# Optimization experiments

Measured on AMD Instinct MI355X. Metric: run time of the kernel, lower is better.

## Reference

```python
import jax, jax.numpy as jnp
import numpy as np

B, C_IN, C_OUT, N = 8, 256, 128, 4096
BN_EPS = 1e-5


def _conv1x1(w, b, t):
    # w: [out, in], t: [B, in, N] -> [B, out, N]
    return jnp.einsum('oc,bcn->bon', w, t) + b[None, :, None]


def setup_inputs() -> dict:
    key = jax.random.key(0)
    ks = jax.random.split(key, 11)
    s_in = 1.0 / np.sqrt(C_IN)
    s_out = 1.0 / np.sqrt(C_OUT)
    return {
        'x': jax.random.normal(ks[0], (B, C_IN, N), dtype=jnp.float32),
        'g_w': jax.random.normal(ks[1], (C_OUT, C_IN), dtype=jnp.float32) * s_in,
        'g_b': jax.random.normal(ks[2], (C_OUT,), dtype=jnp.float32) * s_in,
        'theta_w': jax.random.normal(ks[3], (C_OUT, C_IN), dtype=jnp.float32) * s_in,
        'theta_b': jax.random.normal(ks[4], (C_OUT,), dtype=jnp.float32) * s_in,
        'phi_w': jax.random.normal(ks[5], (C_OUT, C_IN), dtype=jnp.float32) * s_in,
        'phi_b': jax.random.normal(ks[6], (C_OUT,), dtype=jnp.float32) * s_in,
        'W_w': jax.random.normal(ks[7], (C_IN, C_OUT), dtype=jnp.float32) * s_out,
        'W_b': jax.random.normal(ks[8], (C_IN,), dtype=jnp.float32) * s_out,
        'bn_gamma': jax.random.uniform(ks[9], (C_IN,), dtype=jnp.float32),
        'bn_beta': jax.random.normal(ks[10], (C_IN,), dtype=jnp.float32) * 0.1,
    }


def reference(x, g_w, g_b, theta_w, theta_b, phi_w, phi_b, W_w, W_b, bn_gamma, bn_beta):
    n = x.shape[-1]
    g_x = _conv1x1(g_w, g_b, x)          # [B, Co, N]
    theta_x = _conv1x1(theta_w, theta_b, x)  # [B, Co, N]
    phi_x = _conv1x1(phi_w, phi_b, x)        # [B, Co, N]
    # f = theta_x^T @ phi_x, divided by N (no softmax) -> [B, N, N]
    f_div_c = jnp.einsum('bcn,bcm->bnm', theta_x, phi_x) / n
    # y[b,c,n] = sum_m f[b,n,m] * g_x[b,c,m]  -> already permuted to [B, Co, N]
    y = jnp.einsum('bnm,bcm->bcn', f_div_c, g_x)
    w_y = jnp.einsum('oc,bcn->bon', W_w, y) + W_b[None, :, None]  # [B, C_in, N]
    # BatchNorm1d, training mode: stats over (batch, spatial), biased variance
    mean = w_y.mean(axis=(0, 2), keepdims=True)
    var = w_y.var(axis=(0, 2), keepdims=True)
    w_y = (w_y - mean) * jax.lax.rsqrt(var + BN_EPS)
    w_y = w_y * bn_gamma[None, :, None] + bn_beta[None, :, None]
    return w_y + x  # generate=True residual
```

## Files before the change

kernel.cpp:

```cpp
#include <hip/hip_runtime.h>
#include <hip/hip_bf16.h>
#include <stdint.h>

#define BB   8
#define CIN  256
#define COUT 128
#define NN   4096

using f32x4  = __attribute__((ext_vector_type(4))) float;
using bf16x8 = __attribute__((ext_vector_type(8))) __bf16;
using u16x8  = __attribute__((ext_vector_type(8))) unsigned short;

static __device__ __forceinline__ unsigned short f2bf(float f) {
    unsigned int u = __builtin_bit_cast(unsigned int, f);
    u += 0x7FFFu + ((u >> 16) & 1u);
    return (unsigned short)(u >> 16);
}
static __device__ __forceinline__ float bf2f(unsigned short u) {
    return __builtin_bit_cast(float, (unsigned int)u << 16);
}
static __device__ __forceinline__ ushort4 pack4(float a, float b, float c, float d) {
    ushort4 r; r.x=f2bf(a); r.y=f2bf(b); r.z=f2bf(c); r.w=f2bf(d); return r;
}
#define MFMA(a,b,c) __builtin_amdgcn_mfma_f32_16x16x32_bf16((a),(b),(c),0,0,0)

static __device__ __forceinline__ int sw256(int r, int c) { return (r*256 + c) ^ ((r&7)<<3); }
static __device__ __forceinline__ int sw128(int r, int c) { return (r*128 + c) ^ ((r&7)<<3); }

__global__ __launch_bounds__(1024) void kA(
    const float* __restrict__ x,
    unsigned short* __restrict__ Sp, float* __restrict__ Rp)
{
    __shared__ __align__(16) unsigned short SH[65536];
    int bid = blockIdx.x;
    int b = bid >> 4, ch = bid & 15;
    int n0 = ch * 256;
    int t = threadIdx.x, lane = t & 63, wv = t >> 6;
    int lr = lane & 15, lg = lane >> 4;

    const float* xb = x + (size_t)b*CIN*NN + n0 + lane*4;
    #pragma unroll
    for (int g = 0; g < 2; ++g) {
        float4 v[8];
        #pragma unroll
        for (int i = 0; i < 8; ++i) {
            int c = wv*16 + g*8 + i;
            v[i] = *(const float4*)(xb + (size_t)c*NN);
        }
        #pragma unroll
        for (int i = 0; i < 8; ++i) {
            int c = wv*16 + g*8 + i;
            *(ushort4*)&SH[sw256(c, lane*4)] = pack4(v[i].x, v[i].y, v[i].z, v[i].w);
        }
    }
    __syncthreads();

    int wr = wv >> 2, wc = wv & 3;
    f32x4 acc[4][4];
    #pragma unroll
    for (int i = 0; i < 4; ++i)
        #pragma unroll
        for (int j = 0; j < 4; ++j) acc[i][j] = (f32x4){0.f,0.f,0.f,0.f};
    #pragma unroll
    for (int ks = 0; ks < 8; ++ks) {
        bf16x8 af[4], bfr[4];
        #pragma unroll
        for (int mi = 0; mi < 4; ++mi) {
            int row = wr*64 + mi*16 + lr;
            af[mi] = __builtin_bit_cast(bf16x8, *(const u16x8*)&SH[sw256(row, ks*32 + lg*8)]);
        }
        #pragma unroll
        for (int ni = 0; ni < 4; ++ni) {
            int row = wc*64 + ni*16 + lr;
            bfr[ni] = __builtin_bit_cast(bf16x8, *(const u16x8*)&SH[sw256(row, ks*32 + lg*8)]);
        }
        #pragma unroll
        for (int mi = 0; mi < 4; ++mi)
            #pragma unroll
            for (int ni = 0; ni < 4; ++ni)
                acc[mi][ni] = MFMA(af[mi], bfr[ni], acc[mi][ni]);
    }
    if (t < 256) {
        float s = 0.f;
        #pragma unroll
        for (int q = 0; q < 32; ++q) {
            u16x8 vv = *(const u16x8*)&SH[sw256(t, q*8)];
            #pragma unroll
            for (int e = 0; e < 8; ++e) s += bf2f(vv[e]);
        }
        Rp[bid*256 + t] = s;
    }
    __syncthreads();
    #pragma unroll
    for (int mi = 0; mi < 4; ++mi)
        #pragma unroll
        for (int ni = 0; ni < 4; ++ni)
            #pragma unroll
            for (int j = 0; j < 4; ++j) {
                int c1 = wr*64 + mi*16 + lg*4 + j;
                int c2 = wc*64 + ni*16 + lr;
                SH[sw256(c1, c2)] = f2bf(acc[mi][ni][j]);
            }
    __syncthreads();
    unsigned short* dst = Sp + (size_t)bid * 65536;
    #pragma unroll
    for (int i = t; i < 8192; i += 1024) {
        int row = i >> 5, q = i & 31;
        *(u16x8*)(dst + row*256 + ((q ^ (row&7)) * 8)) = *(const u16x8*)&SH[row*256 + q*8];
    }
}

__global__ __launch_bounds__(512) void kR(
    const unsigned short* __restrict__ Sp, const float* __restrict__ Rp,
    const float* __restrict__ Wwf, const float* __restrict__ gwf,
    const float* __restrict__ twf, const float* __restrict__ pwf,
    const float* __restrict__ gbv, const float* __restrict__ pbv, const float* __restrict__ tbv,
    unsigned short* __restrict__ Sbf, float* __restrict__ rv,
    unsigned short* __restrict__ Abf, unsigned short* __restrict__ CmT,
    float* __restrict__ a1, float* __restrict__ c1v, float* __restrict__ p2,
    float* __restrict__ params, float* __restrict__ stats)
{
    __shared__ __align__(16) unsigned short Ls[32768];
    __shared__ __align__(16) unsigned short Rs[32768];
    int bid = blockIdx.x;
    int t = threadIdx.x, lane = t & 63, wv = t >> 6;
    int lr = lane & 15, lg = lane >> 4;

    if (bid < 128) {
        int b = bid >> 4, sl = bid & 15;
        int base = sl*4096 + t*8;
        float s[8] = {0.f,0.f,0.f,0.f,0.f,0.f,0.f,0.f};
        #pragma unroll
        for (int i = 0; i < 16; ++i) {
            u16x8 v = *(const u16x8*)(Sp + (size_t)(b*16 + i)*65536 + base);
            #pragma unroll
            for (int e = 0; e < 8; ++e) s[e] += bf2f(v[e]);
        }
        u16x8 o;
        #pragma unroll
        for (int e = 0; e < 8; ++e) o[e] = f2bf(s[e]);
        *(u16x8*)(Sbf + (size_t)b*65536 + base) = o;
        return;
    }
    if (bid < 136) {
        int b = bid - 128;
        if (t < 256) {
            float s = 0.f;
            #pragma unroll
            for (int i = 0; i < 16; ++i) s += Rp[(b*16 + i)*256 + t];
            rv[b*256 + t] = s;
        }
        return;
    }

    if (bid == 136) {
        for (int i = t; i < 8192; i += 512) {
            int flat = i*4, r = flat >> 7, c = flat & 127;
            float4 f = *(const float4*)(Wwf + flat);
            *(ushort4*)&Ls[sw128(r, c)] = pack4(f.x, f.y, f.z, f.w);
        }
        {
            int c = lane * 4;  int k4 = wv * 4;
            #pragma unroll
            for (int rep = 0; rep < 4; ++rep) {
                int kb = rep*32 + k4;
                float4 f0 = *(const float4*)(gwf + (size_t)(kb+0)*256 + c);
                float4 f1 = *(const float4*)(gwf + (size_t)(kb+1)*256 + c);
                float4 f2 = *(const float4*)(gwf + (size_t)(kb+2)*256 + c);
                float4 f3 = *(const float4*)(gwf + (size_t)(kb+3)*256 + c);
                *(ushort4*)&Rs[sw128(c+0, kb)] = pack4(f0.x, f1.x, f2.x, f3.x);
                *(ushort4*)&Rs[sw128(c+1, kb)] = pack4(f0.y, f1.y, f2.y, f3.y);
                *(ushort4*)&Rs[sw128(c+2, kb)] = pack4(f0.z, f1.z, f2.z, f3.z);
                *(ushort4*)&Rs[sw128(c+3, kb)] = pack4(f0.w, f1.w, f2.w, f3.w);
            }
        }
        if (t < 512) stats[t] = 0.f;
    } else {
        {
            int c = lane * 4;  int k4 = wv * 4;
            #pragma unroll
            for (int rep = 0; rep < 4; ++rep) {
                int kb = rep*32 + k4;
                float4 f0 = *(const float4*)(twf + (size_t)(kb+0)*256 + c);
                float4 f1 = *(const float4*)(twf + (size_t)(kb+1)*256 + c);
                float4 f2 = *(const float4*)(twf + (size_t)(kb+2)*256 + c);
                float4 f3 = *(const float4*)(twf + (size_t)(kb+3)*256 + c);
                *(ushort4*)&Ls[sw128(c+0, kb)] = pack4(f0.x, f1.x, f2.x, f3.x);
                *(ushort4*)&Ls[sw128(c+1, kb)] = pack4(f0.y, f1.y, f2.y, f3.y);
                *(ushort4*)&Ls[sw128(c+2, kb)] = pack4(f0.z, f1.z, f2.z, f3.z);
                *(ushort4*)&Ls[sw128(c+3, kb)] = pack4(f0.w, f1.w, f2.w, f3.w);
                float4 g0 = *(const float4*)(pwf + (size_t)(kb+0)*256 + c);
                float4 g1 = *(const float4*)(pwf + (size_t)(kb+1)*256 + c);
                float4 g2 = *(const float4*)(pwf + (size_t)(kb+2)*256 + c);
                float4 g3 = *(const float4*)(pwf + (size_t)(kb+3)*256 + c);
                *(ushort4*)&Rs[sw128(c+0, kb)] = pack4(g0.x, g1.x, g2.x, g3.x);
                *(ushort4*)&Rs[sw128(c+1, kb)] = pack4(g0.y, g1.y, g2.y, g3.y);
                *(ushort4*)&Rs[sw128(c+2, kb)] = pack4(g0.z, g1.z, g2.z, g3.z);
                *(ushort4*)&Rs[sw128(c+3, kb)] = pack4(g0.w, g1.w, g2.w, g3.w);
            }
        }
    }
    __syncthreads();

    int wr = wv >> 2, wc = wv & 3;
    f32x4 acc[8][4];
    #pragma unroll
    for (int i = 0; i < 8; ++i)
        #pragma unroll
        for (int j = 0; j < 4; ++j) acc[i][j] = (f32x4){0.f,0.f,0.f,0.f};
    #pragma unroll
    for (int ks = 0; ks < 4; ++ks) {
        bf16x8 af[8], bfr[4];
        #pragma unroll
        for (int mi = 0; mi < 8; ++mi) {
            int r = wr*128 + mi*16 + lr;
            af[mi] = __builtin_bit_cast(bf16x8, *(const u16x8*)&Ls[sw128(r, ks*32 + lg*8)]);
        }
        #pragma unroll
        for (int ni = 0; ni < 4; ++ni) {
            int c = wc*64 + ni*16 + lr;
            bfr[ni] = __builtin_bit_cast(bf16x8, *(const u16x8*)&Rs[sw128(c, ks*32 + lg*8)]);
        }
        #pragma unroll
        for (int mi = 0; mi < 8; ++mi)
            #pragma unroll
            for (int ni = 0; ni < 4; ++ni)
                acc[mi][ni] = MFMA(af[mi], bfr[ni], acc[mi][ni]);
    }
    unsigned short* Dst = (bid == 136) ? Abf : CmT;
    #pragma unroll
    for (int mi = 0; mi < 8; ++mi)
        #pragma unroll
        for (int ni = 0; ni < 4; ++ni)
            #pragma unroll
            for (int j = 0; j < 4; ++j) {
                int r = wr*128 + mi*16 + lg*4 + j;
                int c = wc*64 + ni*16 + lr;
                Dst[r*256 + c] = f2bf(acc[mi][ni][j]);
            }

    if (bid == 136) {
        if (t < 256) {
            float s = 0.f;
            #pragma unroll
            for (int q = 0; q < 32; ++q) {
                float4 f = *(const float4*)(Wwf + (size_t)t*128 + q*4);
                s += f.x*gbv[q*4] + f.y*gbv[q*4+1] + f.z*gbv[q*4+2] + f.w*gbv[q*4+3];
            }
            a1[t] = s;
        }
    } else {
        if (t < 256) {
            float s1 = 0.f, s2 = 0.f;
            for (int k = 0; k < 128; ++k) {
                s1 += twf[(size_t)k*256 + t] * pbv[k];
                s2 += pwf[(size_t)k*256 + t] * tbv[k];
            }
            c1v[t] = s1; p2[t] = s2;
        }
        if (t < 64) {
            float v = pbv[t]*tbv[t] + pbv[t+64]*tbv[t+64];
            #pragma unroll
            for (int off = 1; off < 64; off <<= 1) v += __shfl_xor(v, off);
            if (t == 0) params[0] = v;
        }
    }
}

__global__ __launch_bounds__(512) void kE(
    const unsigned short* __restrict__ Sbf, const float* __restrict__ rv,
    const unsigned short* __restrict__ Abf, const unsigned short* __restrict__ CmT,
    const float* __restrict__ a1g, const float* __restrict__ c1vg, const float* __restrict__ p2g,
    const float* __restrict__ params, const float* __restrict__ Wbv,
    unsigned short* __restrict__ Ebf, float* __restrict__ fv, float* __restrict__ stats)
{
    __shared__ __align__(16) unsigned short Ybuf[16384];
    __shared__ __align__(16) unsigned short Ebuf[16384];
    __shared__ float r_l[256], p2_l[256], c1v_l[256], cr[256];
    __shared__ float a1_l[64], ar[64], Yp2[64], er[64], diag_l[64];
    __shared__ float rp2_s;
    int blk = blockIdx.x;
    int b = blk >> 2, obase = (blk & 3) * 64;
    int t = threadIdx.x, lane = t & 63, wv = t >> 6;
    int lr = lane & 15, lg = lane >> 4;
    const float invN = 1.0f/4096.0f;
    const unsigned short* Sb = Sbf + (size_t)b*65536;

    if (t < 256) {
        r_l[t] = rv[b*256 + t];
        p2_l[t] = p2g[t];
        c1v_l[t] = c1vg[t];
    } else if (t < 320) {
        a1_l[t - 256] = a1g[obase + (t - 256)];
    }
    __syncthreads();

    f32x4 acc[4][2];
    #pragma unroll
    for (int i = 0; i < 4; ++i) { acc[i][0] = (f32x4){0,0,0,0}; acc[i][1] = (f32x4){0,0,0,0}; }
    const unsigned short* Arow0 = Abf + (size_t)obase*256;
    #pragma unroll
    for (int ks = 0; ks < 8; ++ks) {
        bf16x8 a4[4], b2[2];
        #pragma unroll
        for (int mi = 0; mi < 4; ++mi)
            a4[mi] = __builtin_bit_cast(bf16x8, *(const u16x8*)(Arow0 + (size_t)(mi*16+lr)*256 + ks*32 + lg*8));
        #pragma unroll
        for (int ni = 0; ni < 2; ++ni)
            b2[ni] = __builtin_bit_cast(bf16x8, *(const u16x8*)(Sb + (size_t)(wv*32+ni*16+lr)*256 + ks*32 + lg*8));
        #pragma unroll
        for (int mi = 0; mi < 4; ++mi)
            #pragma unroll
            for (int ni = 0; ni < 2; ++ni)
                acc[mi][ni] = MFMA(a4[mi], b2[ni], acc[mi][ni]);
    }
    #pragma unroll
    for (int mi = 0; mi < 4; ++mi)
        #pragma unroll
        for (int ni = 0; ni < 2; ++ni)
            #pragma unroll
            for (int j = 0; j < 4; ++j) {
                int ol = mi*16 + lg*4 + j;
                int c2 = wv*32 + ni*16 + lr;
                Ybuf[ol*256 + (c2 ^ ((ol&7)<<3))] = f2bf(acc[mi][ni][j]);
            }
    __syncthreads();

    {
        int row = t >> 3, p8 = t & 7;
        float sA = 0.f, sY = 0.f;
        const unsigned short* Ar = Abf + (size_t)(obase + row)*256 + p8*32;
        #pragma unroll
        for (int q = 0; q < 4; ++q) {
            u16x8 av = *(const u16x8*)(Ar + q*8);
            #pragma unroll
            for (int e = 0; e < 8; ++e) {
                int c = p8*32 + q*8 + e;
                sA += bf2f(av[e]) * r_l[c];
                sY += bf2f(Ybuf[row*256 + (c ^ ((row&7)<<3))]) * p2_l[c];
            }
        }
        sA += __shfl_xor(sA, 1); sA += __shfl_xor(sA, 2); sA += __shfl_xor(sA, 4);
        sY += __shfl_xor(sY, 1); sY += __shfl_xor(sY, 2); sY += __shfl_xor(sY, 4);
        if (p8 == 0) { ar[row] = sA; Yp2[row] = sY; }
    }
    if (t < 256) {
        float s = 0.f;
        const unsigned short* Cr = CmT + (size_t)t*256;
        #pragma unroll
        for (int q = 0; q < 32; ++q) {
            u16x8 v = *(const u16x8*)(Cr + q*8);
            #pragma unroll
            for (int e = 0; e < 8; ++e) s += bf2f(v[e]) * r_l[q*8 + e];
        }
        cr[t] = s;
    }
    if (t < 64) {
        float v = r_l[t*4]*p2_l[t*4] + r_l[t*4+1]*p2_l[t*4+1]
                + r_l[t*4+2]*p2_l[t*4+2] + r_l[t*4+3]*p2_l[t*4+3];
        #pragma unroll
        for (int off = 1; off < 64; off <<= 1) v += __shfl_xor(v, off);
        if (t == 0) rp2_s = v;
    }
    __syncthreads();

    f32x4 accE[4][2];
    #pragma unroll
    for (int i = 0; i < 4; ++i) { accE[i][0] = (f32x4){0,0,0,0}; accE[i][1] = (f32x4){0,0,0,0}; }
    #pragma unroll
    for (int ks = 0; ks < 8; ++ks) {
        bf16x8 a4[4], b2[2];
        #pragma unroll
        for (int mi = 0; mi < 4; ++mi) {
            int ol = mi*16 + lr;
            a4[mi] = __builtin_bit_cast(bf16x8, *(const u16x8*)&Ybuf[ol*256 + ((ks*32 + lg*8) ^ ((ol&7)<<3))]);
        }
        #pragma unroll
        for (int ni = 0; ni < 2; ++ni)
            b2[ni] = __builtin_bit_cast(bf16x8, *(const u16x8*)(CmT + (size_t)(wv*32+ni*16+lr)*256 + ks*32 + lg*8));
        #pragma unroll
        for (int mi = 0; mi < 4; ++mi)
            #pragma unroll
            for (int ni = 0; ni < 2; ++ni)
                accE[mi][ni] = MFMA(a4[mi], b2[ni], accE[mi][ni]);
    }
    unsigned short* Eb = Ebf + (size_t)b*65536;
    #pragma unroll
    for (int mi = 0; mi < 4; ++mi)
        #pragma unroll
        for (int ni = 0; ni < 2; ++ni)
            #pragma unroll
            for (int j = 0; j < 4; ++j) {
                int ol = mi*16 + lg*4 + j;
                int cp = wv*32 + ni*16 + lr;
                float e = accE[mi][ni][j]*invN + a1_l[ol]*invN*cr[cp]
                        + (invN*ar[ol] + a1_l[ol])*c1v_l[cp];
                unsigned short eb = f2bf(e);
                Ebuf[ol*256 + (cp ^ ((ol&7)<<3))] = eb;
                Eb[(size_t)(obase + ol)*256 + cp] = eb;
            }
    __syncthreads();

    float f_reg = 0.f;
    {
        int row = t >> 3, p8 = t & 7;
        float s = 0.f;
        #pragma unroll
        for (int q = 0; q < 4; ++q)
            #pragma unroll
            for (int e = 0; e < 8; ++e) {
                int c = p8*32 + q*8 + e;
                s += bf2f(Ebuf[row*256 + (c ^ ((row&7)<<3))]) * r_l[c];
            }
        s += __shfl_xor(s, 1); s += __shfl_xor(s, 2); s += __shfl_xor(s, 4);
        if (p8 == 0) er[row] = s;
    }
    if (t < 64) {
        diag_l[t] = 0.f;
        float sg = params[0];
        f_reg = invN*(Yp2[t] + a1_l[t]*rp2_s + ar[t]*sg) + a1_l[t]*sg + Wbv[obase + t];
        fv[b*256 + obase + t] = f_reg;
    }
    __syncthreads();

    f32x4 accZ[4][2];
    #pragma unroll
    for (int i = 0; i < 4; ++i) { accZ[i][0] = (f32x4){0,0,0,0}; accZ[i][1] = (f32x4){0,0,0,0}; }
    #pragma unroll
    for (int ks = 0; ks < 8; ++ks) {
        bf16x8 a4[4], b2[2];
        #pragma unroll
        for (int mi = 0; mi < 4; ++mi) {
            int ol = mi*16 + lr;
            a4[mi] = __builtin_bit_cast(bf16x8, *(const u16x8*)&Ebuf[ol*256 + ((ks*32 + lg*8) ^ ((ol&7)<<3))]);
        }
        #pragma unroll
        for (int ni = 0; ni < 2; ++ni)
            b2[ni] = __builtin_bit_cast(bf16x8, *(const u16x8*)(Sb + (size_t)(wv*32+ni*16+lr)*256 + ks*32 + lg*8));
        #pragma unroll
        for (int mi = 0; mi < 4; ++mi)
            #pragma unroll
            for (int ni = 0; ni < 2; ++ni)
                accZ[mi][ni] = MFMA(a4[mi], b2[ni], accZ[mi][ni]);
    }
    #pragma unroll
    for (int mi = 0; mi < 4; ++mi)
        #pragma unroll
        for (int j = 0; j < 4; ++j) {
            int ol = mi*16 + lg*4 + j;
            float s = 0.f;
            #pragma unroll
            for (int ni = 0; ni < 2; ++ni) {
                int c2 = wv*32 + ni*16 + lr;
                s += accZ[mi][ni][j] * bf2f(Ebuf[ol*256 + (c2 ^ ((ol&7)<<3))]);
            }
            s += __shfl_xor(s, 1); s += __shfl_xor(s, 2);
            s += __shfl_xor(s, 4); s += __shfl_xor(s, 8);
            if (lr == 0) atomicAdd(&diag_l[ol], s);
        }
    __syncthreads();

    if (t < 64) {
        int o = obase + t;
        atomicAdd(&stats[o], er[t] + 4096.0f*f_reg);
        atomicAdd(&stats[256 + o], diag_l[t] + 2.0f*f_reg*er[t] + 4096.0f*f_reg*f_reg);
    }
}

__global__ __launch_bounds__(512) void kF(
    const float* __restrict__ x, const unsigned short* __restrict__ Ebf,
    const float* __restrict__ fv, const float* __restrict__ stats,
    const float* __restrict__ gamma, const float* __restrict__ beta,
    float* __restrict__ out)
{
    __shared__ __align__(16) unsigned short Xs[128*256];
    __shared__ float scale_l[256], shift_l[256];
    int b = blockIdx.x >> 5, n0 = (blockIdx.x & 31) * 128;
    int t = threadIdx.x, lane = t & 63, wv = t >> 6, lr = lane & 15, lg = lane >> 4;
    const float inv = 1.0f / 32768.0f;
    if (t < 256) {
        float mu  = stats[t] * inv;
        float var = stats[256 + t] * inv - mu*mu;
        float sc  = gamma[t] * rsqrtf(var + 1e-5f);
        scale_l[t] = sc;
        shift_l[t] = (fv[b*256 + t] - mu) * sc + beta[t];
    }
    {
        int nq = (t & 31) * 4, c0 = (t >> 5) * 4;
        const float* xb = x + (size_t)b*CIN*NN + n0 + nq;
        #pragma unroll
        for (int h = 0; h < 2; ++h) {
            float4 f[8];
            #pragma unroll
            for (int p = 0; p < 2; ++p) {
                int c = (h*2 + p)*64 + c0;
                const float* xp = xb + (size_t)c*NN;
                f[p*4+0] = *(const float4*)(xp);
                f[p*4+1] = *(const float4*)(xp + NN);
                f[p*4+2] = *(const float4*)(xp + 2*NN);
                f[p*4+3] = *(const float4*)(xp + 3*NN);
            }
            #pragma unroll
            for (int p = 0; p < 2; ++p) {
                int c = (h*2 + p)*64 + c0;
                *(ushort4*)&Xs[(nq+0)*256 + (c ^ (((nq+0)&7)<<3))] = pack4(f[p*4].x, f[p*4+1].x, f[p*4+2].x, f[p*4+3].x);
                *(ushort4*)&Xs[(nq+1)*256 + (c ^ (((nq+1)&7)<<3))] = pack4(f[p*4].y, f[p*4+1].y, f[p*4+2].y, f[p*4+3].y);
                *(ushort4*)&Xs[(nq+2)*256 + (c ^ (((nq+2)&7)<<3))] = pack4(f[p*4].z, f[p*4+1].z, f[p*4+2].z, f[p*4+3].z);
                *(ushort4*)&Xs[(nq+3)*256 + (c ^ (((nq+3)&7)<<3))] = pack4(f[p*4].w, f[p*4+1].w, f[p*4+2].w, f[p*4+3].w);
            }
        }
    }
    __syncthreads();

    int wn = wv >> 2, wo = wv & 3;
    int nb = wn*64, ob = wo*64;
    const unsigned short* Eb = Ebf + (size_t)b*65536;
    f32x4 acc[4][4];
    #pragma unroll
    for (int i = 0; i < 4; ++i)
        #pragma unroll
        for (int j = 0; j < 4; ++j) acc[i][j] = (f32x4){0,0,0,0};

    #pragma unroll
    for (int ks = 0; ks < 8; ++ks) {
        bf16x8 xf[4], ef[4];
        #pragma unroll
        for (int ni = 0; ni < 4; ++ni) {
            int n = nb + ni*16 + lr;
            xf[ni] = __builtin_bit_cast(bf16x8, *(const u16x8*)&Xs[(n*256 + ks*32 + lg*8) ^ ((n&7)<<3)]);
        }
        #pragma unroll
        for (int oi = 0; oi < 4; ++oi) {
            int o = ob + oi*16 + lr;
            ef[oi] = __builtin_bit_cast(bf16x8, *(const u16x8*)(Eb + (size_t)o*256 + ks*32 + lg*8));
        }
        #pragma unroll
        for (int oi = 0; oi < 4; ++oi)
            #pragma unroll
            for (int ni = 0; ni < 4; ++ni)
                acc[oi][ni] = MFMA(ef[oi], xf[ni], acc[oi][ni]);
    }

    float* op = out + (size_t)b*CIN*NN + n0;
    #pragma unroll
    for (int oi = 0; oi < 4; ++oi) {
        #pragma unroll
        for (int j = 0; j < 4; ++j) {
            int o = ob + oi*16 + lg*4 + j;
            float sc = scale_l[o], sh = shift_l[o];
            #pragma unroll
            for (int ni = 0; ni < 4; ++ni) {
                int n = nb + ni*16 + lr;
                float val = acc[oi][ni][j]*sc + sh + bf2f(Xs[(n*256 + (o ^ ((n&7)<<3)))]);
                op[(size_t)o*NN + n] = val;
            }
        }
    }
}

extern "C" void kernel_launch(void* const* d_in, const int* in_sizes, int n_in,
                              void* d_out, int out_size, void* d_ws, size_t ws_size,
                              hipStream_t stream)
{
    (void)in_sizes; (void)n_in; (void)out_size; (void)ws_size;
    const float* x     = (const float*)d_in[0];
    const float* gw    = (const float*)d_in[1];
    const float* gb    = (const float*)d_in[2];
    const float* tw    = (const float*)d_in[3];
    const float* tb    = (const float*)d_in[4];
    const float* pw    = (const float*)d_in[5];
    const float* pb    = (const float*)d_in[6];
    const float* Ww    = (const float*)d_in[7];
    const float* Wb    = (const float*)d_in[8];
    const float* gamma = (const float*)d_in[9];
    const float* beta  = (const float*)d_in[10];
    float* out = (float*)d_out;

    char* ws = (char*)d_ws;
    unsigned short* Sp  = (unsigned short*)(ws + 0);
    float* Rp           = (float*)(ws + 16777216);
    unsigned short* Sbf = (unsigned short*)(ws + 16908288);
    float* rv           = (float*)(ws + 17956864);
    unsigned short* Abf = (unsigned short*)(ws + 17965056);
    unsigned short* CmT = (unsigned short*)(ws + 18096128);
    unsigned short* Ebf = (unsigned short*)(ws + 18227200);
    float* fv           = (float*)(ws + 19275776);
    float* a1           = (float*)(ws + 19283968);
    float* c1v          = (float*)(ws + 19284992);
    float* p2           = (float*)(ws + 19286016);
    float* params       = (float*)(ws + 19287040);
    float* stats        = (float*)(ws + 19287104);

    kA<<<128, 1024, 0, stream>>>(x, Sp, Rp);
    kR<<<138, 512,  0, stream>>>(Sp, Rp, Ww, gw, tw, pw, gb, pb, tb,
                                 Sbf, rv, Abf, CmT, a1, c1v, p2, params, stats);
    kE<<<32,  512,  0, stream>>>(Sbf, rv, Abf, CmT, a1, c1v, p2, params, Wb, Ebf, fv, stats);
    kF<<<256, 512,  0, stream>>>(x, Ebf, fv, stats, gamma, beta, out);
}
```

Before: 91.38 us.

## Halve per-block N tiles in kA and kF to double grid size

kA now handles 128 spatial columns per 512-thread block (256 blocks), computing the 256x256 Gram partial with an 8-wave layout and writing it back in two half-passes through a halved LDS buffer. kF processes 64 columns per block over 512 blocks with half the accumulators. The intent is to fill more CUs on the 256-CU device, since the old 128- and 256-block grids left many CUs idle. In exchange kA writes twice as many partial Gram matrices (double the Sp workspace), and kR's reduction reads 32 partials instead of 16, which adds memory traffic.

```diff
diff --git a/kernel.cpp b/kernel.cpp
--- a/kernel.cpp
+++ b/kernel.cpp
@@ -27,86 +27,91 @@
 static __device__ __forceinline__ int sw256(int r, int c) { return (r*256 + c) ^ ((r&7)<<3); }
 static __device__ __forceinline__ int sw128(int r, int c) { return (r*128 + c) ^ ((r&7)<<3); }
 
-__global__ __launch_bounds__(1024) void kA(
+__global__ __launch_bounds__(512) void kA(
     const float* __restrict__ x,
     unsigned short* __restrict__ Sp, float* __restrict__ Rp)
 {
-    __shared__ __align__(16) unsigned short SH[65536];
+    __shared__ __align__(16) unsigned short SH[32768];
     int bid = blockIdx.x;
-    int b = bid >> 4, ch = bid & 15;
-    int n0 = ch * 256;
+    int b = bid >> 5, ch = bid & 31;
+    int n0 = ch * 128;
     int t = threadIdx.x, lane = t & 63, wv = t >> 6;
     int lr = lane & 15, lg = lane >> 4;
 
-    const float* xb = x + (size_t)b*CIN*NN + n0 + lane*4;
-    #pragma unroll
-    for (int g = 0; g < 2; ++g) {
-        float4 v[8];
-        #pragma unroll
-        for (int i = 0; i < 8; ++i) {
-            int c = wv*16 + g*8 + i;
-            v[i] = *(const float4*)(xb + (size_t)c*NN);
-        }
-        #pragma unroll
-        for (int i = 0; i < 8; ++i) {
-            int c = wv*16 + g*8 + i;
-            *(ushort4*)&SH[sw256(c, lane*4)] = pack4(v[i].x, v[i].y, v[i].z, v[i].w);
-        }
-    }
-    __syncthreads();
-
-    int wr = wv >> 2, wc = wv & 3;
-    f32x4 acc[4][4];
+    {
+        int n4 = (t & 31) * 4;
+        int c0 = t >> 5;
+        const float* xb = x + (size_t)b*CIN*NN + n0 + n4;
+        float4 v[16];
+        #pragma unroll
+        for (int i = 0; i < 16; ++i)
+            v[i] = *(const float4*)(xb + (size_t)(c0 + i*16)*NN);
+        #pragma unroll
+        for (int i = 0; i < 16; ++i) {
+            int c = c0 + i*16;
+            *(ushort4*)&SH[sw128(c, n4)] = pack4(v[i].x, v[i].y, v[i].z, v[i].w);
+        }
+    }
+    __syncthreads();
+
+    int wr = wv >> 1, wc = wv & 1;
+    f32x4 acc[4][8];
     #pragma unroll
     for (int i = 0; i < 4; ++i)
         #pragma unroll
-        for (int j = 0; j < 4; ++j) acc[i][j] = (f32x4){0.f,0.f,0.f,0.f};
-    #pragma unroll
-    for (int ks = 0; ks < 8; ++ks) {
-        bf16x8 af[4], bfr[4];
+        for (int j = 0; j < 8; ++j) acc[i][j] = (f32x4){0.f,0.f,0.f,0.f};
+    #pragma unroll
+    for (int ks = 0; ks < 4; ++ks) {
+        bf16x8 af[4], bfr[8];
         #pragma unroll
         for (int mi = 0; mi < 4; ++mi) {
             int row = wr*64 + mi*16 + lr;
-            af[mi] = __builtin_bit_cast(bf16x8, *(const u16x8*)&SH[sw256(row, ks*32 + lg*8)]);
-        }
-        #pragma unroll
-        for (int ni = 0; ni < 4; ++ni) {
-            int row = wc*64 + ni*16 + lr;
-            bfr[ni] = __builtin_bit_cast(bf16x8, *(const u16x8*)&SH[sw256(row, ks*32 + lg*8)]);
+            af[mi] = __builtin_bit_cast(bf16x8, *(const u16x8*)&SH[sw128(row, ks*32 + lg*8)]);
+        }
+        #pragma unroll
+        for (int ni = 0; ni < 8; ++ni) {
+            int row = wc*128 + ni*16 + lr;
+            bfr[ni] = __builtin_bit_cast(bf16x8, *(const u16x8*)&SH[sw128(row, ks*32 + lg*8)]);
         }
         #pragma unroll
         for (int mi = 0; mi < 4; ++mi)
             #pragma unroll
-            for (int ni = 0; ni < 4; ++ni)
+            for (int ni = 0; ni < 8; ++ni)
                 acc[mi][ni] = MFMA(af[mi], bfr[ni], acc[mi][ni]);
     }
     if (t < 256) {
         float s = 0.f;
         #pragma unroll
-        for (int q = 0; q < 32; ++q) {
-            u16x8 vv = *(const u16x8*)&SH[sw256(t, q*8)];
+        for (int q = 0; q < 16; ++q) {
+            u16x8 vv = *(const u16x8*)&SH[sw128(t, q*8)];
             #pragma unroll
             for (int e = 0; e < 8; ++e) s += bf2f(vv[e]);
         }
         Rp[bid*256 + t] = s;
     }
-    __syncthreads();
-    #pragma unroll
-    for (int mi = 0; mi < 4; ++mi)
-        #pragma unroll
-        for (int ni = 0; ni < 4; ++ni)
-            #pragma unroll
-            for (int j = 0; j < 4; ++j) {
-                int c1 = wr*64 + mi*16 + lg*4 + j;
-                int c2 = wc*64 + ni*16 + lr;
-                SH[sw256(c1, c2)] = f2bf(acc[mi][ni][j]);
-            }
-    __syncthreads();
+
     unsigned short* dst = Sp + (size_t)bid * 65536;
     #pragma unroll
-    for (int i = t; i < 8192; i += 1024) {
-        int row = i >> 5, q = i & 31;
-        *(u16x8*)(dst + row*256 + ((q ^ (row&7)) * 8)) = *(const u16x8*)&SH[row*256 + q*8];
+    for (int p = 0; p < 2; ++p) {
+        __syncthreads();
+        if (wc == p) {
+            #pragma unroll
+            for (int mi = 0; mi < 4; ++mi)
+                #pragma unroll
+                for (int ni = 0; ni < 8; ++ni)
+                    #pragma unroll
+                    for (int j = 0; j < 4; ++j) {
+                        int c1 = wr*64 + mi*16 + lg*4 + j;
+                        int c2l = ni*16 + lr;
+                        SH[sw128(c1, c2l)] = f2bf(acc[mi][ni][j]);
+                    }
+        }
+        __syncthreads();
+        #pragma unroll
+        for (int i = t; i < 4096; i += 512) {
+            int row = i >> 4, q = i & 15;
+            *(u16x8*)(dst + row*256 + p*128 + ((q ^ (row&7)) * 8)) = *(const u16x8*)&SH[row*128 + q*8];
+        }
     }
 }
 
@@ -131,8 +136,8 @@
         int base = sl*4096 + t*8;
         float s[8] = {0.f,0.f,0.f,0.f,0.f,0.f,0.f,0.f};
         #pragma unroll
-        for (int i = 0; i < 16; ++i) {
-            u16x8 v = *(const u16x8*)(Sp + (size_t)(b*16 + i)*65536 + base);
+        for (int i = 0; i < 32; ++i) {
+            u16x8 v = *(const u16x8*)(Sp + (size_t)(b*32 + i)*65536 + base);
             #pragma unroll
             for (int e = 0; e < 8; ++e) s[e] += bf2f(v[e]);
         }
@@ -147,7 +152,7 @@
         if (t < 256) {
             float s = 0.f;
             #pragma unroll
-            for (int i = 0; i < 16; ++i) s += Rp[(b*16 + i)*256 + t];
+            for (int i = 0; i < 32; ++i) s += Rp[(b*32 + i)*256 + t];
             rv[b*256 + t] = s;
         }
         return;
@@ -473,9 +478,9 @@
     const float* __restrict__ gamma, const float* __restrict__ beta,
     float* __restrict__ out)
 {
-    __shared__ __align__(16) unsigned short Xs[128*256];
+    __shared__ __align__(16) unsigned short Xs[64*256];
     __shared__ float scale_l[256], shift_l[256];
-    int b = blockIdx.x >> 5, n0 = (blockIdx.x & 31) * 128;
+    int b = blockIdx.x >> 6, n0 = (blockIdx.x & 63) * 64;
     int t = threadIdx.x, lane = t & 63, wv = t >> 6, lr = lane & 15, lg = lane >> 4;
     const float inv = 1.0f / 32768.0f;
     if (t < 256) {
@@ -486,46 +491,42 @@
         shift_l[t] = (fv[b*256 + t] - mu) * sc + beta[t];
     }
     {
-        int nq = (t & 31) * 4, c0 = (t >> 5) * 4;
-        const float* xb = x + (size_t)b*CIN*NN + n0 + nq;
-        #pragma unroll
-        for (int h = 0; h < 2; ++h) {
-            float4 f[8];
-            #pragma unroll
-            for (int p = 0; p < 2; ++p) {
-                int c = (h*2 + p)*64 + c0;
-                const float* xp = xb + (size_t)c*NN;
-                f[p*4+0] = *(const float4*)(xp);
-                f[p*4+1] = *(const float4*)(xp + NN);
-                f[p*4+2] = *(const float4*)(xp + 2*NN);
-                f[p*4+3] = *(const float4*)(xp + 3*NN);
-            }
-            #pragma unroll
-            for (int p = 0; p < 2; ++p) {
-                int c = (h*2 + p)*64 + c0;
-                *(ushort4*)&Xs[(nq+0)*256 + (c ^ (((nq+0)&7)<<3))] = pack4(f[p*4].x, f[p*4+1].x, f[p*4+2].x, f[p*4+3].x);
-                *(ushort4*)&Xs[(nq+1)*256 + (c ^ (((nq+1)&7)<<3))] = pack4(f[p*4].y, f[p*4+1].y, f[p*4+2].y, f[p*4+3].y);
-                *(ushort4*)&Xs[(nq+2)*256 + (c ^ (((nq+2)&7)<<3))] = pack4(f[p*4].z, f[p*4+1].z, f[p*4+2].z, f[p*4+3].z);
-                *(ushort4*)&Xs[(nq+3)*256 + (c ^ (((nq+3)&7)<<3))] = pack4(f[p*4].w, f[p*4+1].w, f[p*4+2].w, f[p*4+3].w);
-            }
+        int n4 = (t & 15) * 4;
+        int cb = (t >> 4) * 4;
+        const float* xb = x + (size_t)b*CIN*NN + n0 + n4;
+        float4 f[8];
+        #pragma unroll
+        for (int p = 0; p < 2; ++p) {
+            int c = p*128 + cb;
+            const float* xp = xb + (size_t)c*NN;
+            f[p*4+0] = *(const float4*)(xp);
+            f[p*4+1] = *(const float4*)(xp + NN);
+            f[p*4+2] = *(const float4*)(xp + 2*NN);
+            f[p*4+3] = *(const float4*)(xp + 3*NN);
+        }
+        #pragma unroll
+        for (int p = 0; p < 2; ++p) {
+            int c = p*128 + cb;
+            *(ushort4*)&Xs[(n4+0)*256 + (c ^ (((n4+0)&7)<<3))] = pack4(f[p*4].x, f[p*4+1].x, f[p*4+2].x, f[p*4+3].x);
+            *(ushort4*)&Xs[(n4+1)*256 + (c ^ (((n4+1)&7)<<3))] = pack4(f[p*4].y, f[p*4+1].y, f[p*4+2].y, f[p*4+3].y);
+            *(ushort4*)&Xs[(n4+2)*256 + (c ^ (((n4+2)&7)<<3))] = pack4(f[p*4].z, f[p*4+1].z, f[p*4+2].z, f[p*4+3].z);
+            *(ushort4*)&Xs[(n4+3)*256 + (c ^ (((n4+3)&7)<<3))] = pack4(f[p*4].w, f[p*4+1].w, f[p*4+2].w, f[p*4+3].w);
         }
     }
     __syncthreads();
 
     int wn = wv >> 2, wo = wv & 3;
-    int nb = wn*64, ob = wo*64;
+    int nb = wn*32, ob = wo*64;
     const unsigned short* Eb = Ebf + (size_t)b*65536;
-    f32x4 acc[4][4];
-    #pragma unroll
-    for (int i = 0; i < 4; ++i)
-        #pragma unroll
-        for (int j = 0; j < 4; ++j) acc[i][j] = (f32x4){0,0,0,0};
+    f32x4 acc[4][2];
+    #pragma unroll
+    for (int i = 0; i < 4; ++i) { acc[i][0] = (f32x4){0,0,0,0}; acc[i][1] = (f32x4){0,0,0,0}; }
 
     #pragma unroll
     for (int ks = 0; ks < 8; ++ks) {
-        bf16x8 xf[4], ef[4];
-        #pragma unroll
-        for (int ni = 0; ni < 4; ++ni) {
+        bf16x8 xf[2], ef[4];
+        #pragma unroll
+        for (int ni = 0; ni < 2; ++ni) {
             int n = nb + ni*16 + lr;
             xf[ni] = __builtin_bit_cast(bf16x8, *(const u16x8*)&Xs[(n*256 + ks*32 + lg*8) ^ ((n&7)<<3)]);
         }
@@ -537,7 +538,7 @@
         #pragma unroll
         for (int oi = 0; oi < 4; ++oi)
             #pragma unroll
-            for (int ni = 0; ni < 4; ++ni)
+            for (int ni = 0; ni < 2; ++ni)
                 acc[oi][ni] = MFMA(ef[oi], xf[ni], acc[oi][ni]);
     }
 
@@ -549,7 +550,7 @@
             int o = ob + oi*16 + lg*4 + j;
             float sc = scale_l[o], sh = shift_l[o];
             #pragma unroll
-            for (int ni = 0; ni < 4; ++ni) {
+            for (int ni = 0; ni < 2; ++ni) {
                 int n = nb + ni*16 + lr;
                 float val = acc[oi][ni][j]*sc + sh + bf2f(Xs[(n*256 + (o ^ ((n&7)<<3)))]);
                 op[(size_t)o*NN + n] = val;
@@ -578,22 +579,22 @@
 
     char* ws = (char*)d_ws;
     unsigned short* Sp  = (unsigned short*)(ws + 0);
-    float* Rp           = (float*)(ws + 16777216);
-    unsigned short* Sbf = (unsigned short*)(ws + 16908288);
-    float* rv           = (float*)(ws + 17956864);
-    unsigned short* Abf = (unsigned short*)(ws + 17965056);
-    unsigned short* CmT = (unsigned short*)(ws + 18096128);
-    unsigned short* Ebf = (unsigned short*)(ws + 18227200);
-    float* fv           = (float*)(ws + 19275776);
-    float* a1           = (float*)(ws + 19283968);
-    float* c1v          = (float*)(ws + 19284992);
-    float* p2           = (float*)(ws + 19286016);
-    float* params       = (float*)(ws + 19287040);
-    float* stats        = (float*)(ws + 19287104);
-
-    kA<<<128, 1024, 0, stream>>>(x, Sp, Rp);
-    kR<<<138, 512,  0, stream>>>(Sp, Rp, Ww, gw, tw, pw, gb, pb, tb,
-                                 Sbf, rv, Abf, CmT, a1, c1v, p2, params, stats);
-    kE<<<32,  512,  0, stream>>>(Sbf, rv, Abf, CmT, a1, c1v, p2, params, Wb, Ebf, fv, stats);
-    kF<<<256, 512,  0, stream>>>(x, Ebf, fv, stats, gamma, beta, out);
-}
+    float* Rp           = (float*)(ws + 33554432);
+    unsigned short* Sbf = (unsigned short*)(ws + 33816576);
+    float* rv           = (float*)(ws + 34865152);
+    unsigned short* Abf = (unsigned short*)(ws + 34873344);
+    unsigned short* CmT = (unsigned short*)(ws + 35004416);
+    unsigned short* Ebf = (unsigned short*)(ws + 35135488);
+    float* fv           = (float*)(ws + 36184064);
+    float* a1           = (float*)(ws + 36192256);
+    float* c1v          = (float*)(ws + 36193280);
+    float* p2           = (float*)(ws + 36194304);
+    float* params       = (float*)(ws + 36195328);
+    float* stats        = (float*)(ws + 36195392);
+
+    kA<<<256, 512, 0, stream>>>(x, Sp, Rp);
+    kR<<<138, 512, 0, stream>>>(Sp, Rp, Ww, gw, tw, pw, gb, pb, tb,
+                                Sbf, rv, Abf, CmT, a1, c1v, p2, params, stats);
+    kE<<<32,  512, 0, stream>>>(Sbf, rv, Abf, CmT, a1, c1v, p2, params, Wb, Ebf, fv, stats);
+    kF<<<512, 512, 0, stream>>>(x, Ebf, fv, stats, gamma, beta, out);
+}
```

Measured after the change: 100.9 us. 10.4% more time.
